# Performance work log

Measured on AMD Instinct MI355X. Metric: run time of the kernel, lower is better.

## Reference

```python
import jax, jax.numpy as jnp
import numpy as np

B, V, J, NPOSE, NBETAS = 512, 6890, 24, 46, 10
PARENTS = np.array([-1, 0, 1, 2, 3, 4, 0, 6, 7, 8, 9, 0, 11, 12, 12, 14, 15, 16, 17, 12, 19, 20, 21, 22])

def _euler_xyz(e):
    x, y, z = e
    cx, sx = np.cos(x), np.sin(x)
    cy, sy = np.cos(y), np.sin(y)
    cz, sz = np.cos(z), np.sin(z)
    Rx = np.array([[1, 0, 0], [0, cx, -sx], [0, sx, cx]])
    Ry = np.array([[cy, 0, sy], [0, 1, 0], [-sy, 0, cy]])
    Rz = np.array([[cz, -sz, 0], [sz, cz, 0], [0, 0, 1]])
    return Rx @ Ry @ Rz

def _pin(e):
    return (_euler_xyz(e) @ np.array([0.0, 0.0, 1.0])).tolist()

JOINT_AXES = [
    [[0, 0, 1], [1, 0, 0], [0, 1, 0]],
    [[0, 0, 1], [1, 0, 0], [0, 1, 0]],
    [[0, 0, -1]],
    [_pin([0.175895, -0.105208, 0.0186622])],
    [_pin([-1.76818999, 0.906223, 1.8196])],
    [_pin([-3.14158999, 0.619901, 0])],
    [[0, 0, 1], [-1, 0, 0], [0, -1, 0]],
    [[0, 0, -1]],
    [_pin([0.175895, -0.105208, 0.0186622])],
    [_pin([1.76818999, -0.906223, 1.8196])],
    [_pin([-3.14158999, -0.619901, 0])],
    [[1, 0, 0], [0, 0, 1], [0, 1, 0]],
    [[1, 0, 0], [0, 0, 1], [0, 1, 0]],
    [[1, 0, 0], [0, 0, 1], [0, 1, 0]],
    [[0, 1, 0], [0, 0, -1], [-1, 0, 0]],
    [[1, 0, 0], [0, 1, 0], [0, 0, 1]],
    [[0.0494, 0.0366, 0.99810825]],
    [[-0.01716099, 0.99266564, -0.11966796]],
    [[1, 0, 0], [0, 0, -1]],
    [[0, 1, 0], [0, 0, 1], [1, 0, 0]],
    [[1, 0, 0], [0, 1, 0], [0, 0, 1]],
    [[-0.0494, -0.0366, 0.99810825]],
    [[0.01716099, -0.99266564, -0.11966796]],
    [[-1, 0, 0], [0, 0, -1]],
]

def _build_axes():
    all_axes, ridx, d = [], [], 0
    for axes in JOINT_AXES:
        n = len(axes)
        for ax in axes:
            a = np.array(ax, dtype=np.float32)
            nn = np.linalg.norm(a)
            if nn > 1e-6 and abs(nn - 1.0) > 1e-6:
                a = a / nn
            all_axes.append(a)
        if n == 1:
            ridx.append([d, NPOSE, NPOSE])
        elif n == 2:
            ridx.append([d, d + 1, NPOSE])
        else:
            ridx.append([d, d + 1, d + 2])
        d += n
    all_axes.append(np.zeros(3, np.float32))
    return np.stack(all_axes).astype(np.float32), np.array(ridx)

_AXES_NP, RIDX = _build_axes()  # [47,3], [24,3]
ALL_AXES = jnp.asarray(_AXES_NP)

def rodrigues(v):
    # axis-angle [...,3] -> rotation matrix [...,3,3], Rodrigues formula
    theta = jnp.maximum(jnp.linalg.norm(v, axis=-1, keepdims=True), 1e-8)
    r = v / theta
    rx, ry, rz = r[..., 0], r[..., 1], r[..., 2]
    z = jnp.zeros_like(rx)
    K = jnp.stack([jnp.stack([z, -rz, ry], -1),
                   jnp.stack([rz, z, -rx], -1),
                   jnp.stack([-ry, rx, z], -1)], -2)
    s = jnp.sin(theta)[..., None]
    c = jnp.cos(theta)[..., None]
    return jnp.eye(3, dtype=v.dtype) + s * K + (1 - c) * (K @ K)


def setup_inputs() -> dict:
    key = jax.random.key(0)
    ks = jax.random.split(key, 10)
    betas = jax.random.normal(ks[0], (B, NBETAS), jnp.float32)
    poses = 0.3 * jax.random.normal(ks[1], (B, NPOSE), jnp.float32)
    trans = 0.1 * jax.random.normal(ks[2], (B, 3), jnp.float32)
    v_template = 0.3 * jax.random.normal(ks[3], (V, 3), jnp.float32)
    shapedirs = 0.01 * jax.random.normal(ks[4], (V, 3, NBETAS), jnp.float32)
    posedirs = 0.01 * jax.random.normal(ks[5], (V, 3, 9 * (J - 1)), jnp.float32)
    jr = jax.random.uniform(ks[6], (J, V), jnp.float32)
    J_regressor = jr / jr.sum(-1, keepdims=True)
    sw = jax.random.uniform(ks[7], (V, J), jnp.float32) ** 8  # sparse-ish skinning weights
    skin_weights = sw / sw.sum(-1, keepdims=True)
    apose_R = rodrigues(0.2 * jax.random.normal(ks[8], (J, 3), jnp.float32))
    per_joint_rot = rodrigues(0.2 * jax.random.normal(ks[9], (J, 3), jnp.float32))
    return {"betas": betas, "poses": poses, "trans": trans, "v_template": v_template,
            "shapedirs": shapedirs, "posedirs": posedirs, "J_regressor": J_regressor,
            "skin_weights": skin_weights, "apose_R": apose_R, "per_joint_rot": per_joint_rot}


def reference(betas, poses, trans, v_template, shapedirs, posedirs, J_regressor, skin_weights, apose_R, per_joint_rot):
    b = poses.shape[0]
    # per-DOF axis-angle rotations; index NPOSE is the padded identity DOF (zero axis)
    q = jnp.concatenate([poses, jnp.zeros((b, 1), poses.dtype)], -1)       # [B,47]
    Rd = rodrigues(q[..., None] * ALL_AXES)                                 # [B,47,3,3]
    Rj = Rd[:, RIDX[:, 0]] @ Rd[:, RIDX[:, 1]] @ Rd[:, RIDX[:, 2]]          # [B,24,3,3]
    # express in anatomical joint frames, compose with A-pose rest rotation
    P = per_joint_rot[None]                                                 # [1,24,3,3]
    R_local = apose_R[None] @ (P @ Rj @ jnp.swapaxes(P, -1, -2))            # [B,24,3,3]

    v_shaped = v_template + jnp.einsum('vck,bk->bvc', shapedirs, betas)     # [B,V,3]
    Jloc = jnp.einsum('jv,bvc->bjc', J_regressor, v_shaped)                 # [B,24,3]

    # forward kinematics along the fixed 24-joint tree
    G_R = [R_local[:, 0]]
    G_t = [Jloc[:, 0]]
    for j in range(1, J):
        p = int(PARENTS[j])
        G_R.append(G_R[p] @ R_local[:, j])
        G_t.append(G_t[p] + jnp.einsum('bmn,bn->bm', G_R[p], Jloc[:, j] - Jloc[:, p]))
    GR = jnp.stack(G_R, 1)                                                  # [B,24,3,3]
    Gt = jnp.stack(G_t, 1)                                                  # [B,24,3]

    # pose blend shapes from non-root joint rotations
    pose_feat = (Rj[:, 1:] - jnp.eye(3, dtype=Rj.dtype)).reshape(b, 9 * (J - 1))
    v_posed = v_shaped + jnp.einsum('vcp,bp->bvc', posedirs, pose_feat)     # [B,V,3]

    # unpose rest joints, then linear blend skinning
    A_t = Gt - jnp.einsum('bjmn,bjn->bjm', GR, Jloc)                        # [B,24,3]
    T_R = jnp.einsum('vj,bjmn->bvmn', skin_weights, GR)                     # [B,V,3,3]
    T_t = jnp.einsum('vj,bjm->bvm', skin_weights, A_t)                      # [B,V,3]
    verts = jnp.einsum('bvmn,bvn->bvm', T_R, v_posed) + T_t + trans[:, None]
    return verts
```

## Files before the change

kernel.cpp:

```cpp
#include <hip/hip_runtime.h>
#include <cstdint>
#include <cstddef>

#define B_   512
#define V_   6890
#define VP   6912
#define NJ   24
#define KF   224
#define NP   46
#define NVT  432
#define NBT  32
#define NKT  7

typedef float f32x4 __attribute__((ext_vector_type(4)));
typedef short s16x8 __attribute__((ext_vector_type(8)));

__device__ __forceinline__ unsigned short f2bf(float f) {
  unsigned int u = __float_as_uint(f);
  u = (u + 0x7FFFu + ((u >> 16) & 1u)) >> 16;
  return (unsigned short)u;
}
__device__ __forceinline__ float bf2f(unsigned short h) {
  return __uint_as_float(((unsigned int)h) << 16);
}

__constant__ float c_axes[47][3] = {
  { 0.f, 0.f, 1.f}, { 1.f, 0.f, 0.f}, { 0.f, 1.f, 0.f},
  { 0.f, 0.f, 1.f}, { 1.f, 0.f, 0.f}, { 0.f, 1.f, 0.f},
  { 0.f, 0.f,-1.f},
  {-0.10501402f,-0.17402183f, 0.97912636f},
  { 0.78718019f, 0.60474702f,-0.12094817f},
  { 0.58095459f, 0.00000217f,-0.81393598f},
  { 0.f, 0.f, 1.f}, {-1.f, 0.f, 0.f}, { 0.f,-1.f, 0.f},
  { 0.f, 0.f,-1.f},
  {-0.10501402f,-0.17402183f, 0.97912636f},
  {-0.78718019f,-0.60474702f,-0.12094817f},
  {-0.58095459f, 0.00000217f,-0.81393598f},
  { 1.f, 0.f, 0.f}, { 0.f, 0.f, 1.f}, { 0.f, 1.f, 0.f},
  { 1.f, 0.f, 0.f}, { 0.f, 0.f, 1.f}, { 0.f, 1.f, 0.f},
  { 1.f, 0.f, 0.f}, { 0.f, 0.f, 1.f}, { 0.f, 1.f, 0.f},
  { 0.f, 1.f, 0.f}, { 0.f, 0.f,-1.f}, {-1.f, 0.f, 0.f},
  { 1.f, 0.f, 0.f}, { 0.f, 1.f, 0.f}, { 0.f, 0.f, 1.f},
  { 0.0494f, 0.0366f, 0.99810825f},
  {-0.01716099f, 0.99266564f,-0.11966796f},
  { 1.f, 0.f, 0.f}, { 0.f, 0.f,-1.f},
  { 0.f, 1.f, 0.f}, { 0.f, 0.f, 1.f}, { 1.f, 0.f, 0.f},
  { 1.f, 0.f, 0.f}, { 0.f, 1.f, 0.f}, { 0.f, 0.f, 1.f},
  {-0.0494f,-0.0366f, 0.99810825f},
  { 0.01716099f,-0.99266564f,-0.11966796f},
  {-1.f, 0.f, 0.f}, { 0.f, 0.f,-1.f},
  { 0.f, 0.f, 0.f}
};
__constant__ int c_ridx[24][3] = {
  {0,1,2},{3,4,5},{6,46,46},{7,46,46},{8,46,46},{9,46,46},
  {10,11,12},{13,46,46},{14,46,46},{15,46,46},{16,46,46},
  {17,18,19},{20,21,22},{23,24,25},{26,27,28},{29,30,31},
  {32,46,46},{33,46,46},{34,35,46},{36,37,38},{39,40,41},
  {42,46,46},{43,46,46},{44,45,46}
};
__constant__ int c_par[24] = {-1,0,1,2,3,4,0,6,7,8,9,0,11,12,12,14,15,16,17,12,19,20,21,22};

__device__ __forceinline__ void mm3(const float* A, const float* Bm, float* C) {
#pragma unroll
  for (int i = 0; i < 3; ++i)
#pragma unroll
    for (int j = 0; j < 3; ++j)
      C[i*3+j] = A[i*3+0]*Bm[0+j] + A[i*3+1]*Bm[3+j] + A[i*3+2]*Bm[6+j];
}
__device__ __forceinline__ void mm3_bt(const float* A, const float* Bm, float* C) {
#pragma unroll
  for (int i = 0; i < 3; ++i)
#pragma unroll
    for (int j = 0; j < 3; ++j)
      C[i*3+j] = A[i*3+0]*Bm[j*3+0] + A[i*3+1]*Bm[j*3+1] + A[i*3+2]*Bm[j*3+2];
}

__global__ __launch_bounds__(256) void k0_prep(const float* __restrict__ posed,
                                               const float* __restrict__ sd,
                                               const float* __restrict__ vt,
                                               const float* __restrict__ sw,
                                               unsigned short* __restrict__ pdm,
                                               unsigned short* __restrict__ smf,
                                               float* __restrict__ jts) {
  const int lane = threadIdx.x & 63;
  if (blockIdx.x < 2268) {
    int tile = blockIdx.x * 4 + (threadIdx.x >> 6);
    int kt = tile % NKT;
    int vtg = (tile / NKT) % NVT;
    int c  = tile / (NKT * NVT);
    int v  = vtg*16 + (lane & 15);
    int kb = kt*32 + (lane >> 4)*8;
    unsigned short vals[8];
#pragma unroll
    for (int j = 0; j < 8; ++j) {
      int k = kb + j;
      float f = 0.f;
      if (v < V_) {
        if (k < 207)       f = posed[(v*3 + c)*207 + k];
        else if (k < 217)  f = sd[(v*3 + c)*10 + (k - 207)];
        else if (k == 217) f = vt[v*3 + c];
      }
      vals[j] = f2bf(f);
    }
    *(uint4*)(pdm + (size_t)tile*512 + lane*8) = *(const uint4*)vals;
  } else {
    if (blockIdx.x == 2268) {
      for (int i = threadIdx.x; i < 24*33; i += 256) jts[i] = 0.f;
    }
    int tile = (blockIdx.x - 2268) * 4 + (threadIdx.x >> 6);
    int slot = tile & 1;
    int vtg  = tile >> 1;
    int v = vtg*16 + (lane & 15);
    int j0 = (lane >> 4) * 8;
    unsigned short vals[8];
#pragma unroll
    for (int jj = 0; jj < 8; ++jj) {
      int j = j0 + jj;
      float s = (v < V_ && j < NJ) ? sw[v*NJ + j] : 0.f;
      unsigned short hi = f2bf(s);
      vals[jj] = slot ? f2bf(s - bf2f(hi)) : hi;
    }
    *(uint4*)(smf + (size_t)tile*512 + lane*8) = *(const uint4*)vals;
  }
}

__global__ __launch_bounds__(256) void k1_jts(const float* __restrict__ jreg,
                                              const float* __restrict__ vt,
                                              const float* __restrict__ sd,
                                              float* __restrict__ jts) {
  const int j = blockIdx.x % 24;
  const int chunk = blockIdx.x / 24;
  const int v0 = chunk * 864;
  const int v1 = (v0 + 864 < V_) ? v0 + 864 : V_;
  float acc[3][11];
#pragma unroll
  for (int c = 0; c < 3; ++c)
#pragma unroll
    for (int i = 0; i < 11; ++i) acc[c][i] = 0.f;
  for (int v = v0 + threadIdx.x; v < v1; v += 256) {
    float wgt = jreg[j*V_ + v];
#pragma unroll
    for (int c = 0; c < 3; ++c) {
      acc[c][0] += wgt * vt[v*3 + c];
      const float* s = sd + (v*3 + c)*10;
#pragma unroll
      for (int k = 0; k < 10; ++k) acc[c][1+k] += wgt * s[k];
    }
  }
#pragma unroll
  for (int c = 0; c < 3; ++c)
#pragma unroll
    for (int i = 0; i < 11; ++i)
#pragma unroll
      for (int o = 32; o > 0; o >>= 1) acc[c][i] += __shfl_xor(acc[c][i], o, 64);
  __shared__ float red[4][33];
  int wid = threadIdx.x >> 6, ln = threadIdx.x & 63;
  if (ln == 0) {
#pragma unroll
    for (int c = 0; c < 3; ++c)
#pragma unroll
      for (int i = 0; i < 11; ++i) red[wid][c*11+i] = acc[c][i];
  }
  __syncthreads();
  if (threadIdx.x < 33) {
    float s = red[0][threadIdx.x] + red[1][threadIdx.x] +
              red[2][threadIdx.x] + red[3][threadIdx.x];
    atomicAdd(&jts[j*33 + threadIdx.x], s);
  }
}

__global__ void k2_pose(const float* __restrict__ poses, const float* __restrict__ betas,
                        const float* __restrict__ trans, const float* __restrict__ apose,
                        const float* __restrict__ pjr, const float* __restrict__ jts,
                        float* __restrict__ Fw, float* __restrict__ Mw) {
  const int b = blockIdx.x;
  const int t = threadIdx.x;
  __shared__ float Rd[47][9];
  __shared__ float Rj[24][9];
  __shared__ float Rl[24][9];
  __shared__ float jl[24][3];
  __shared__ float G[24][12];

  if (t < 47) {
    float q  = (t < NP) ? poses[b*NP + t] : 0.f;
    float ax = c_axes[t][0], ay = c_axes[t][1], az = c_axes[t][2];
    float s = sinf(q), cq = cosf(q);
    float u = 1.f - cq;
    Rd[t][0] = u*ax*ax + cq;   Rd[t][1] = u*ax*ay - s*az; Rd[t][2] = u*ax*az + s*ay;
    Rd[t][3] = u*ax*ay + s*az; Rd[t][4] = u*ay*ay + cq;   Rd[t][5] = u*ay*az - s*ax;
    Rd[t][6] = u*ax*az - s*ay; Rd[t][7] = u*ay*az + s*ax; Rd[t][8] = u*az*az + cq;
  }
  if (t < NJ) {
    const float* jr = jts + t*33;
#pragma unroll
    for (int c = 0; c < 3; ++c) {
      float a = jr[c*11];
#pragma unroll
      for (int k = 0; k < 10; ++k) a += jr[c*11 + 1 + k] * betas[b*10 + k];
      jl[t][c] = a;
    }
  }
  __syncthreads();
  if (t < NJ) {
    float C1[9], C2[9];
    const int r0 = c_ridx[t][0], r1 = c_ridx[t][1], r2 = c_ridx[t][2];
    mm3(&Rd[r0][0], &Rd[r1][0], C1);
    mm3(C1, &Rd[r2][0], C2);
#pragma unroll
    for (int e = 0; e < 9; ++e) Rj[t][e] = C2[e];
    float P[9], Ap[9];
#pragma unroll
    for (int e = 0; e < 9; ++e) { P[e] = pjr[t*9 + e]; Ap[e] = apose[t*9 + e]; }
    mm3(P, C2, C1);
    mm3_bt(C1, P, C2);
    mm3(Ap, C2, C1);
#pragma unroll
    for (int e = 0; e < 9; ++e) Rl[t][e] = C1[e];
  }
  __syncthreads();
  if (t == 0) {
#pragma unroll
    for (int e = 0; e < 9; ++e) G[0][e] = Rl[0][e];
    G[0][9] = jl[0][0]; G[0][10] = jl[0][1]; G[0][11] = jl[0][2];
    for (int j = 1; j < NJ; ++j) {
      int p = c_par[j];
      float R[9];
      mm3(&G[p][0], &Rl[j][0], R);
#pragma unroll
      for (int e = 0; e < 9; ++e) G[j][e] = R[e];
      float d0 = jl[j][0]-jl[p][0], d1 = jl[j][1]-jl[p][1], d2 = jl[j][2]-jl[p][2];
      G[j][9]  = G[p][9]  + G[p][0]*d0 + G[p][1]*d1 + G[p][2]*d2;
      G[j][10] = G[p][10] + G[p][3]*d0 + G[p][4]*d1 + G[p][5]*d2;
      G[j][11] = G[p][11] + G[p][6]*d0 + G[p][7]*d1 + G[p][8]*d2;
    }
  }
  __syncthreads();
  if (t < NJ) {
    float tx = trans[b*3+0], ty = trans[b*3+1], tz = trans[b*3+2];
    float a0 = G[t][9]  - (G[t][0]*jl[t][0] + G[t][1]*jl[t][1] + G[t][2]*jl[t][2]) + tx;
    float a1 = G[t][10] - (G[t][3]*jl[t][0] + G[t][4]*jl[t][1] + G[t][5]*jl[t][2]) + ty;
    float a2 = G[t][11] - (G[t][6]*jl[t][0] + G[t][7]*jl[t][1] + G[t][8]*jl[t][2]) + tz;
    float* m = Mw + b*288 + t*12;
#pragma unroll
    for (int e = 0; e < 9; ++e) m[e] = G[t][e];
    m[9] = a0; m[10] = a1; m[11] = a2;
  }
  for (int k = t; k < KF; k += 64) {
    float val;
    if (k < 207) {
      int jj = k / 9 + 1;
      int e  = k % 9;
      val = Rj[jj][e] - ((e == 0 || e == 4 || e == 8) ? 1.f : 0.f);
    } else if (k < 217) val = betas[b*10 + (k - 207)];
    else if (k == 217)  val = 1.f;
    else                val = 0.f;
    Fw[b*KF + k] = val;
  }
}

__global__ __launch_bounds__(256) void k2bc_frag(const float* __restrict__ Fw,
                                                 const float* __restrict__ Mw,
                                                 unsigned short* __restrict__ fmf,
                                                 unsigned short* __restrict__ mmf) {
  const int lane = threadIdx.x & 63;
  if (blockIdx.x < 56) {
    int tile = blockIdx.x * 4 + (threadIdx.x >> 6);
    int kt = tile % NKT;
    int bt = tile / NKT;
    int b  = bt*16 + (lane & 15);
    int kb = kt*32 + (lane >> 4)*8;
    unsigned short vals[8];
#pragma unroll
    for (int j = 0; j < 8; ++j) vals[j] = f2bf(Fw[b*KF + kb + j]);
    *(uint4*)(fmf + (size_t)tile*512 + lane*8) = *(const uint4*)vals;
  } else {
    int tile = (blockIdx.x - 56) * 4 + (threadIdx.x >> 6);
    int slot = tile & 1;
    int bt   = (tile >> 1) % NBT;
    int e    = tile / (2*NBT);
    int b  = bt*16 + (lane & 15);
    int j0 = (lane >> 4) * 8;
    unsigned short vals[8];
#pragma unroll
    for (int jj = 0; jj < 8; ++jj) {
      int j = j0 + jj;
      float f = (j < NJ) ? Mw[b*288 + j*12 + e] : 0.f;
      unsigned short hi = f2bf(f);
      vals[jj] = slot ? f2bf(f - bf2f(hi)) : hi;
    }
    *(uint4*)(mmf + (size_t)tile*512 + lane*8) = *(const uint4*)vals;
  }
}

__global__ __launch_bounds__(512) void k3_verts(
    const unsigned short* __restrict__ pdm,
    const unsigned short* __restrict__ fmf,
    const unsigned short* __restrict__ smf,
    const unsigned short* __restrict__ mmf,
    float* __restrict__ out)
{
  const int wg   = (blockIdx.x & 7) * 54 + (blockIdx.x >> 3);
  const int bt_blk = wg & 7;
  const int vt_blk = wg >> 3;
  const int t    = threadIdx.x;
  const int lane = t & 63;
  const int w    = t >> 6;
  const int wv   = w >> 1, wb = w & 1;
  const int vtg0 = vt_blk*8 + wv*2;
  const int btg0 = bt_blk*4 + wb*2;

  f32x4 acc1[2][2][3];
#pragma unroll
  for (int vs = 0; vs < 2; ++vs)
#pragma unroll
    for (int bs = 0; bs < 2; ++bs)
#pragma unroll
      for (int c = 0; c < 3; ++c) acc1[vs][bs][c] = (f32x4){0.f,0.f,0.f,0.f};

#pragma unroll 1
  for (int kt = 0; kt < NKT; ++kt) {
    s16x8 fa[2], pb[2][3];
#pragma unroll
    for (int bs = 0; bs < 2; ++bs)
      fa[bs] = *(const s16x8*)(fmf + ((size_t)(btg0+bs)*NKT + kt)*512 + lane*8);
#pragma unroll
    for (int vs = 0; vs < 2; ++vs)
#pragma unroll
      for (int c = 0; c < 3; ++c)
        pb[vs][c] = *(const s16x8*)(pdm + (((size_t)c*NVT + vtg0+vs)*NKT + kt)*512 + lane*8);
#pragma unroll
    for (int vs = 0; vs < 2; ++vs)
#pragma unroll
      for (int bs = 0; bs < 2; ++bs)
#pragma unroll
        for (int c = 0; c < 3; ++c)
          acc1[vs][bs][c] = __builtin_amdgcn_mfma_f32_16x16x32_bf16(fa[bs], pb[vs][c], acc1[vs][bs][c], 0, 0, 0);
  }

  s16x8 sh[2], sl[2];
#pragma unroll
  for (int vs = 0; vs < 2; ++vs) {
    sh[vs] = *(const s16x8*)(smf + ((size_t)(vtg0+vs)*2 + 0)*512 + lane*8);
    sl[vs] = *(const s16x8*)(smf + ((size_t)(vtg0+vs)*2 + 1)*512 + lane*8);
  }

  f32x4 vo[2][2][3];
#pragma unroll
  for (int vs = 0; vs < 2; ++vs)
#pragma unroll
    for (int bs = 0; bs < 2; ++bs)
#pragma unroll
      for (int m = 0; m < 3; ++m) vo[vs][bs][m] = (f32x4){0.f,0.f,0.f,0.f};

#pragma unroll
  for (int e = 0; e < 12; ++e) {
    s16x8 mh[2], ml[2];
#pragma unroll
    for (int bs = 0; bs < 2; ++bs) {
      mh[bs] = *(const s16x8*)(mmf + (((size_t)e*NBT + btg0+bs)*2 + 0)*512 + lane*8);
      ml[bs] = *(const s16x8*)(mmf + (((size_t)e*NBT + btg0+bs)*2 + 1)*512 + lane*8);
    }
#pragma unroll
    for (int vs = 0; vs < 2; ++vs)
#pragma unroll
      for (int bs = 0; bs < 2; ++bs) {
        f32x4 tmp = (f32x4){0.f,0.f,0.f,0.f};
        tmp = __builtin_amdgcn_mfma_f32_16x16x32_bf16(mh[bs], sh[vs], tmp, 0, 0, 0);
        tmp = __builtin_amdgcn_mfma_f32_16x16x32_bf16(ml[bs], sh[vs], tmp, 0, 0, 0);
        tmp = __builtin_amdgcn_mfma_f32_16x16x32_bf16(mh[bs], sl[vs], tmp, 0, 0, 0);
        if (e < 9) vo[vs][bs][e/3] += tmp * acc1[vs][bs][e%3];
        else       vo[vs][bs][e-9] += tmp;
      }
  }

#pragma unroll
  for (int vs = 0; vs < 2; ++vs) {
    const int v = (vtg0+vs)*16 + (lane & 15);
    if (v < V_) {
#pragma unroll
      for (int bs = 0; bs < 2; ++bs) {
        const int b0 = (btg0+bs)*16 + (lane >> 4)*4;
#pragma unroll
        for (int q = 0; q < 4; ++q) {
          float* op = out + ((size_t)(b0 + q)*V_ + v)*3;
          op[0] = vo[vs][bs][0][q];
          op[1] = vo[vs][bs][1][q];
          op[2] = vo[vs][bs][2][q];
        }
      }
    }
  }
}

extern "C" void kernel_launch(void* const* d_in, const int* in_sizes, int n_in,
                              void* d_out, int out_size, void* d_ws, size_t ws_size,
                              hipStream_t stream) {
  (void)in_sizes; (void)n_in; (void)out_size; (void)ws_size;
  const float* betas      = (const float*)d_in[0];
  const float* poses      = (const float*)d_in[1];
  const float* trans      = (const float*)d_in[2];
  const float* v_template = (const float*)d_in[3];
  const float* shapedirs  = (const float*)d_in[4];
  const float* posedirs   = (const float*)d_in[5];
  const float* jreg       = (const float*)d_in[6];
  const float* skinw      = (const float*)d_in[7];
  const float* apose      = (const float*)d_in[8];
  const float* pjr        = (const float*)d_in[9];
  float* out = (float*)d_out;
  float* ws  = (float*)d_ws;

  unsigned short* pdm = (unsigned short*)ws;
  unsigned short* fmf = (unsigned short*)(ws + 2322432);
  unsigned short* smf = (unsigned short*)(ws + 2379776);
  unsigned short* mmf = (unsigned short*)(ws + 2600960);
  float* Fw  = ws + 2797568;
  float* Mw  = ws + 2912256;
  float* jts = ws + 3059712;

  hipLaunchKernelGGL(k0_prep, dim3(2484), dim3(256), 0, stream,
                     posedirs, shapedirs, v_template, skinw, pdm, smf, jts);
  hipLaunchKernelGGL(k1_jts, dim3(24*8), dim3(256), 0, stream,
                     jreg, v_template, shapedirs, jts);
  hipLaunchKernelGGL(k2_pose, dim3(B_), dim3(64), 0, stream,
                     poses, betas, trans, apose, pjr, jts, Fw, Mw);
  hipLaunchKernelGGL(k2bc_frag, dim3(248), dim3(256), 0, stream, Fw, Mw, fmf, mmf);
  hipLaunchKernelGGL(k3_verts, dim3(432), dim3(512), 0, stream,
                     pdm, fmf, smf, mmf, out);
}
```

Baseline: 70.93 us.

## Fuse prep stages into three kernels and build fragments directly in pose kernel

Moves the joint-regressor reduction into the prep kernel: 24 blocks each reduce one joint across all vertices, so the zero-init and atomics go away. The pose kernel now handles 16 batch items per 1024-thread block and writes the bf16 MFMA fragments for the features and transforms straight from shared memory. This removes the Fw/Mw global round trip and the separate fragment kernel. It cuts launches from five to three, at the cost of a long serial per-joint reduction in 24 blocks and only 32 blocks for the pose stage.

Measured after the change: 100.6 us. +41.9%, slower.

```diff
diff --git a/kernel.cpp b/kernel.cpp
--- a/kernel.cpp
+++ b/kernel.cpp
@@ -75,21 +75,58 @@
       C[i*3+j] = A[i*3+0]*Bm[j*3+0] + A[i*3+1]*Bm[j*3+1] + A[i*3+2]*Bm[j*3+2];
 }
 
-__global__ __launch_bounds__(256) void k0_prep(const float* __restrict__ posed,
+__global__ __launch_bounds__(256) void kA_prep(const float* __restrict__ posed,
                                                const float* __restrict__ sd,
                                                const float* __restrict__ vt,
                                                const float* __restrict__ sw,
+                                               const float* __restrict__ jreg,
                                                unsigned short* __restrict__ pdm,
                                                unsigned short* __restrict__ smf,
                                                float* __restrict__ jts) {
+  const int bid  = blockIdx.x;
   const int lane = threadIdx.x & 63;
-  if (blockIdx.x < 2268) {
-    int tile = blockIdx.x * 4 + (threadIdx.x >> 6);
-    int kt = tile % NKT;
+  if (bid < 24) {
+    const int j = bid;
+    float acc[3][11];
+#pragma unroll
+    for (int c = 0; c < 3; ++c)
+#pragma unroll
+      for (int i = 0; i < 11; ++i) acc[c][i] = 0.f;
+    for (int v = threadIdx.x; v < V_; v += 256) {
+      float wgt = jreg[j*V_ + v];
+#pragma unroll
+      for (int c = 0; c < 3; ++c) {
+        acc[c][0] += wgt * vt[v*3 + c];
+        const float* s = sd + (v*3 + c)*10;
+#pragma unroll
+        for (int k = 0; k < 10; ++k) acc[c][1+k] += wgt * s[k];
+      }
+    }
+#pragma unroll
+    for (int c = 0; c < 3; ++c)
+#pragma unroll
+      for (int i = 0; i < 11; ++i)
+#pragma unroll
+        for (int o = 32; o > 0; o >>= 1) acc[c][i] += __shfl_xor(acc[c][i], o, 64);
+    __shared__ float red[4][33];
+    int wid = threadIdx.x >> 6;
+    if (lane == 0) {
+#pragma unroll
+      for (int c = 0; c < 3; ++c)
+#pragma unroll
+        for (int i = 0; i < 11; ++i) red[wid][c*11+i] = acc[c][i];
+    }
+    __syncthreads();
+    if (threadIdx.x < 33)
+      jts[j*33 + threadIdx.x] = red[0][threadIdx.x] + red[1][threadIdx.x] +
+                                red[2][threadIdx.x] + red[3][threadIdx.x];
+  } else if (bid < 2292) {
+    int tile = (bid - 24) * 4 + (threadIdx.x >> 6);
+    int kt  = tile % NKT;
     int vtg = (tile / NKT) % NVT;
-    int c  = tile / (NKT * NVT);
-    int v  = vtg*16 + (lane & 15);
-    int kb = kt*32 + (lane >> 4)*8;
+    int c   = tile / (NKT * NVT);
+    int v   = vtg*16 + (lane & 15);
+    int kb  = kt*32 + (lane >> 4)*8;
     unsigned short vals[8];
 #pragma unroll
     for (int j = 0; j < 8; ++j) {
@@ -104,13 +141,10 @@
     }
     *(uint4*)(pdm + (size_t)tile*512 + lane*8) = *(const uint4*)vals;
   } else {
-    if (blockIdx.x == 2268) {
-      for (int i = threadIdx.x; i < 24*33; i += 256) jts[i] = 0.f;
-    }
-    int tile = (blockIdx.x - 2268) * 4 + (threadIdx.x >> 6);
+    int tile = (bid - 2292) * 4 + (threadIdx.x >> 6);
     int slot = tile & 1;
     int vtg  = tile >> 1;
-    int v = vtg*16 + (lane & 15);
+    int v  = vtg*16 + (lane & 15);
     int j0 = (lane >> 4) * 8;
     unsigned short vals[8];
 #pragma unroll
@@ -124,175 +158,132 @@
   }
 }
 
-__global__ __launch_bounds__(256) void k1_jts(const float* __restrict__ jreg,
-                                              const float* __restrict__ vt,
-                                              const float* __restrict__ sd,
-                                              float* __restrict__ jts) {
-  const int j = blockIdx.x % 24;
-  const int chunk = blockIdx.x / 24;
-  const int v0 = chunk * 864;
-  const int v1 = (v0 + 864 < V_) ? v0 + 864 : V_;
-  float acc[3][11];
-#pragma unroll
-  for (int c = 0; c < 3; ++c)
-#pragma unroll
-    for (int i = 0; i < 11; ++i) acc[c][i] = 0.f;
-  for (int v = v0 + threadIdx.x; v < v1; v += 256) {
-    float wgt = jreg[j*V_ + v];
-#pragma unroll
-    for (int c = 0; c < 3; ++c) {
-      acc[c][0] += wgt * vt[v*3 + c];
-      const float* s = sd + (v*3 + c)*10;
-#pragma unroll
-      for (int k = 0; k < 10; ++k) acc[c][1+k] += wgt * s[k];
-    }
-  }
-#pragma unroll
-  for (int c = 0; c < 3; ++c)
-#pragma unroll
-    for (int i = 0; i < 11; ++i)
-#pragma unroll
-      for (int o = 32; o > 0; o >>= 1) acc[c][i] += __shfl_xor(acc[c][i], o, 64);
-  __shared__ float red[4][33];
-  int wid = threadIdx.x >> 6, ln = threadIdx.x & 63;
-  if (ln == 0) {
-#pragma unroll
-    for (int c = 0; c < 3; ++c)
-#pragma unroll
-      for (int i = 0; i < 11; ++i) red[wid][c*11+i] = acc[c][i];
-  }
-  __syncthreads();
-  if (threadIdx.x < 33) {
-    float s = red[0][threadIdx.x] + red[1][threadIdx.x] +
-              red[2][threadIdx.x] + red[3][threadIdx.x];
-    atomicAdd(&jts[j*33 + threadIdx.x], s);
-  }
-}
-
-__global__ void k2_pose(const float* __restrict__ poses, const float* __restrict__ betas,
-                        const float* __restrict__ trans, const float* __restrict__ apose,
-                        const float* __restrict__ pjr, const float* __restrict__ jts,
-                        float* __restrict__ Fw, float* __restrict__ Mw) {
-  const int b = blockIdx.x;
-  const int t = threadIdx.x;
-  __shared__ float Rd[47][9];
-  __shared__ float Rj[24][9];
-  __shared__ float Rl[24][9];
-  __shared__ float jl[24][3];
-  __shared__ float G[24][12];
-
-  if (t < 47) {
-    float q  = (t < NP) ? poses[b*NP + t] : 0.f;
-    float ax = c_axes[t][0], ay = c_axes[t][1], az = c_axes[t][2];
+__global__ __launch_bounds__(1024) void kB_pose(const float* __restrict__ poses,
+                                                const float* __restrict__ betas,
+                                                const float* __restrict__ trans,
+                                                const float* __restrict__ apose,
+                                                const float* __restrict__ pjr,
+                                                const float* __restrict__ jts,
+                                                unsigned short* __restrict__ fmf,
+                                                unsigned short* __restrict__ mmf) {
+  __shared__ float RdG[16][423];
+  __shared__ float Rj[16][216];
+  __shared__ float Rl[16][216];
+  __shared__ float jl[16][24][3];
+  const int t  = threadIdx.x;
+  const int bl = t >> 6;
+  const int tl = t & 63;
+  const int bt = blockIdx.x;
+  const int b  = bt*16 + bl;
+
+  float* Rd = RdG[bl];
+  if (tl < 47) {
+    float q  = (tl < NP) ? poses[b*NP + tl] : 0.f;
+    float ax = c_axes[tl][0], ay = c_axes[tl][1], az = c_axes[tl][2];
     float s = sinf(q), cq = cosf(q);
     float u = 1.f - cq;
-    Rd[t][0] = u*ax*ax + cq;   Rd[t][1] = u*ax*ay - s*az; Rd[t][2] = u*ax*az + s*ay;
-    Rd[t][3] = u*ax*ay + s*az; Rd[t][4] = u*ay*ay + cq;   Rd[t][5] = u*ay*az - s*ax;
-    Rd[t][6] = u*ax*az - s*ay; Rd[t][7] = u*ay*az + s*ax; Rd[t][8] = u*az*az + cq;
-  }
-  if (t < NJ) {
-    const float* jr = jts + t*33;
+    Rd[tl*9+0] = u*ax*ax + cq;   Rd[tl*9+1] = u*ax*ay - s*az; Rd[tl*9+2] = u*ax*az + s*ay;
+    Rd[tl*9+3] = u*ax*ay + s*az; Rd[tl*9+4] = u*ay*ay + cq;   Rd[tl*9+5] = u*ay*az - s*ax;
+    Rd[tl*9+6] = u*ax*az - s*ay; Rd[tl*9+7] = u*ay*az + s*ax; Rd[tl*9+8] = u*az*az + cq;
+  }
+  if (tl < NJ) {
+    const float* jr = jts + tl*33;
 #pragma unroll
     for (int c = 0; c < 3; ++c) {
       float a = jr[c*11];
 #pragma unroll
       for (int k = 0; k < 10; ++k) a += jr[c*11 + 1 + k] * betas[b*10 + k];
-      jl[t][c] = a;
+      jl[bl][tl][c] = a;
     }
   }
   __syncthreads();
-  if (t < NJ) {
+  if (tl < NJ) {
     float C1[9], C2[9];
-    const int r0 = c_ridx[t][0], r1 = c_ridx[t][1], r2 = c_ridx[t][2];
-    mm3(&Rd[r0][0], &Rd[r1][0], C1);
-    mm3(C1, &Rd[r2][0], C2);
-#pragma unroll
-    for (int e = 0; e < 9; ++e) Rj[t][e] = C2[e];
+    const int r0 = c_ridx[tl][0], r1 = c_ridx[tl][1], r2 = c_ridx[tl][2];
+    mm3(&Rd[r0*9], &Rd[r1*9], C1);
+    mm3(C1, &Rd[r2*9], C2);
+#pragma unroll
+    for (int e = 0; e < 9; ++e) Rj[bl][tl*9+e] = C2[e];
     float P[9], Ap[9];
 #pragma unroll
-    for (int e = 0; e < 9; ++e) { P[e] = pjr[t*9 + e]; Ap[e] = apose[t*9 + e]; }
+    for (int e = 0; e < 9; ++e) { P[e] = pjr[tl*9 + e]; Ap[e] = apose[tl*9 + e]; }
     mm3(P, C2, C1);
     mm3_bt(C1, P, C2);
     mm3(Ap, C2, C1);
 #pragma unroll
-    for (int e = 0; e < 9; ++e) Rl[t][e] = C1[e];
+    for (int e = 0; e < 9; ++e) Rl[bl][tl*9+e] = C1[e];
   }
   __syncthreads();
-  if (t == 0) {
-#pragma unroll
-    for (int e = 0; e < 9; ++e) G[0][e] = Rl[0][e];
-    G[0][9] = jl[0][0]; G[0][10] = jl[0][1]; G[0][11] = jl[0][2];
+  if (tl == 0) {
+    float* G = RdG[bl];
+#pragma unroll
+    for (int e = 0; e < 9; ++e) G[e] = Rl[bl][e];
+    G[9] = jl[bl][0][0]; G[10] = jl[bl][0][1]; G[11] = jl[bl][0][2];
     for (int j = 1; j < NJ; ++j) {
       int p = c_par[j];
       float R[9];
-      mm3(&G[p][0], &Rl[j][0], R);
-#pragma unroll
-      for (int e = 0; e < 9; ++e) G[j][e] = R[e];
-      float d0 = jl[j][0]-jl[p][0], d1 = jl[j][1]-jl[p][1], d2 = jl[j][2]-jl[p][2];
-      G[j][9]  = G[p][9]  + G[p][0]*d0 + G[p][1]*d1 + G[p][2]*d2;
-      G[j][10] = G[p][10] + G[p][3]*d0 + G[p][4]*d1 + G[p][5]*d2;
-      G[j][11] = G[p][11] + G[p][6]*d0 + G[p][7]*d1 + G[p][8]*d2;
+      mm3(&G[p*12], &Rl[bl][j*9], R);
+#pragma unroll
+      for (int e = 0; e < 9; ++e) G[j*12+e] = R[e];
+      float d0 = jl[bl][j][0]-jl[bl][p][0], d1 = jl[bl][j][1]-jl[bl][p][1], d2 = jl[bl][j][2]-jl[bl][p][2];
+      G[j*12+ 9] = G[p*12+ 9] + G[p*12+0]*d0 + G[p*12+1]*d1 + G[p*12+2]*d2;
+      G[j*12+10] = G[p*12+10] + G[p*12+3]*d0 + G[p*12+4]*d1 + G[p*12+5]*d2;
+      G[j*12+11] = G[p*12+11] + G[p*12+6]*d0 + G[p*12+7]*d1 + G[p*12+8]*d2;
     }
   }
   __syncthreads();
-  if (t < NJ) {
+  if (tl < NJ) {
+    float* G = RdG[bl];
+    float jx = jl[bl][tl][0], jy = jl[bl][tl][1], jz = jl[bl][tl][2];
     float tx = trans[b*3+0], ty = trans[b*3+1], tz = trans[b*3+2];
-    float a0 = G[t][9]  - (G[t][0]*jl[t][0] + G[t][1]*jl[t][1] + G[t][2]*jl[t][2]) + tx;
-    float a1 = G[t][10] - (G[t][3]*jl[t][0] + G[t][4]*jl[t][1] + G[t][5]*jl[t][2]) + ty;
-    float a2 = G[t][11] - (G[t][6]*jl[t][0] + G[t][7]*jl[t][1] + G[t][8]*jl[t][2]) + tz;
-    float* m = Mw + b*288 + t*12;
-#pragma unroll
-    for (int e = 0; e < 9; ++e) m[e] = G[t][e];
-    m[9] = a0; m[10] = a1; m[11] = a2;
-  }
-  for (int k = t; k < KF; k += 64) {
-    float val;
-    if (k < 207) {
-      int jj = k / 9 + 1;
-      int e  = k % 9;
-      val = Rj[jj][e] - ((e == 0 || e == 4 || e == 8) ? 1.f : 0.f);
-    } else if (k < 217) val = betas[b*10 + (k - 207)];
-    else if (k == 217)  val = 1.f;
-    else                val = 0.f;
-    Fw[b*KF + k] = val;
-  }
-}
-
-__global__ __launch_bounds__(256) void k2bc_frag(const float* __restrict__ Fw,
-                                                 const float* __restrict__ Mw,
-                                                 unsigned short* __restrict__ fmf,
-                                                 unsigned short* __restrict__ mmf) {
-  const int lane = threadIdx.x & 63;
-  if (blockIdx.x < 56) {
-    int tile = blockIdx.x * 4 + (threadIdx.x >> 6);
-    int kt = tile % NKT;
-    int bt = tile / NKT;
-    int b  = bt*16 + (lane & 15);
-    int kb = kt*32 + (lane >> 4)*8;
+    float a0 = G[tl*12+ 9] - (G[tl*12+0]*jx + G[tl*12+1]*jy + G[tl*12+2]*jz) + tx;
+    float a1 = G[tl*12+10] - (G[tl*12+3]*jx + G[tl*12+4]*jy + G[tl*12+5]*jz) + ty;
+    float a2 = G[tl*12+11] - (G[tl*12+6]*jx + G[tl*12+7]*jy + G[tl*12+8]*jz) + tz;
+    G[tl*12+ 9] = a0; G[tl*12+10] = a1; G[tl*12+11] = a2;
+  }
+  __syncthreads();
+
+  if (t < 448) {
+    int kt = t >> 6;
+    int ln = t & 63;
+    int bl2 = ln & 15;
+    int kb  = kt*32 + (ln >> 4)*8;
     unsigned short vals[8];
 #pragma unroll
-    for (int j = 0; j < 8; ++j) vals[j] = f2bf(Fw[b*KF + kb + j]);
-    *(uint4*)(fmf + (size_t)tile*512 + lane*8) = *(const uint4*)vals;
-  } else {
-    int tile = (blockIdx.x - 56) * 4 + (threadIdx.x >> 6);
-    int slot = tile & 1;
-    int bt   = (tile >> 1) % NBT;
-    int e    = tile / (2*NBT);
-    int b  = bt*16 + (lane & 15);
-    int j0 = (lane >> 4) * 8;
+    for (int j = 0; j < 8; ++j) {
+      int k = kb + j;
+      float val;
+      if (k < 207) {
+        int jj = k / 9 + 1, e = k % 9;
+        val = Rj[bl2][jj*9+e] - ((e == 0 || e == 4 || e == 8) ? 1.f : 0.f);
+      } else if (k < 217) val = betas[(bt*16 + bl2)*10 + (k - 207)];
+      else if (k == 217)  val = 1.f;
+      else                val = 0.f;
+      vals[j] = f2bf(val);
+    }
+    *(uint4*)(fmf + ((size_t)bt*NKT + kt)*512 + ln*8) = *(const uint4*)vals;
+  }
+  for (int task = t; task < 1536; task += 1024) {
+    int e    = task >> 7;
+    int rem  = task & 127;
+    int slot = rem >> 6;
+    int ln   = rem & 63;
+    int bl2  = ln & 15;
+    int j0   = (ln >> 4) * 8;
+    const float* G = RdG[bl2];
     unsigned short vals[8];
 #pragma unroll
     for (int jj = 0; jj < 8; ++jj) {
       int j = j0 + jj;
-      float f = (j < NJ) ? Mw[b*288 + j*12 + e] : 0.f;
+      float f = (j < NJ) ? G[j*12 + e] : 0.f;
       unsigned short hi = f2bf(f);
       vals[jj] = slot ? f2bf(f - bf2f(hi)) : hi;
     }
-    *(uint4*)(mmf + (size_t)tile*512 + lane*8) = *(const uint4*)vals;
-  }
-}
-
-__global__ __launch_bounds__(512) void k3_verts(
+    *(uint4*)(mmf + (((size_t)e*NBT + bt)*2 + slot)*512 + ln*8) = *(const uint4*)vals;
+  }
+}
+
+__global__ __launch_bounds__(512) void kC_verts(
     const unsigned short* __restrict__ pdm,
     const unsigned short* __restrict__ fmf,
     const unsigned short* __restrict__ smf,
@@ -413,17 +404,12 @@
   unsigned short* fmf = (unsigned short*)(ws + 2322432);
   unsigned short* smf = (unsigned short*)(ws + 2379776);
   unsigned short* mmf = (unsigned short*)(ws + 2600960);
-  float* Fw  = ws + 2797568;
-  float* Mw  = ws + 2912256;
-  float* jts = ws + 3059712;
-
-  hipLaunchKernelGGL(k0_prep, dim3(2484), dim3(256), 0, stream,
-                     posedirs, shapedirs, v_template, skinw, pdm, smf, jts);
-  hipLaunchKernelGGL(k1_jts, dim3(24*8), dim3(256), 0, stream,
-                     jreg, v_template, shapedirs, jts);
-  hipLaunchKernelGGL(k2_pose, dim3(B_), dim3(64), 0, stream,
-                     poses, betas, trans, apose, pjr, jts, Fw, Mw);
-  hipLaunchKernelGGL(k2bc_frag, dim3(248), dim3(256), 0, stream, Fw, Mw, fmf, mmf);
-  hipLaunchKernelGGL(k3_verts, dim3(432), dim3(512), 0, stream,
+  float* jts = ws + 2797568;
+
+  hipLaunchKernelGGL(kA_prep, dim3(2508), dim3(256), 0, stream,
+                     posedirs, shapedirs, v_template, skinw, jreg, pdm, smf, jts);
+  hipLaunchKernelGGL(kB_pose, dim3(32), dim3(1024), 0, stream,
+                     poses, betas, trans, apose, pjr, jts, fmf, mmf);
+  hipLaunchKernelGGL(kC_verts, dim3(432), dim3(512), 0, stream,
                      pdm, fmf, smf, mmf, out);
 }
```
